# Kernel optimization log

Hardware: AMD Instinct MI355X
Metric: run time of the kernel (lower is better)

The kernel has to match this reference:

```python
import jax, jax.numpy as jnp
import numpy as np

WS = 8
HEADS = 12


def _dwconv(x, w, b):
    # x: (N, C, H, W); w: (C, 1, 3, 3) depthwise, zero pad 1
    y = jax.lax.conv_general_dilated(
        x, w, window_strides=(1, 1), padding=((1, 1), (1, 1)),
        dimension_numbers=("NCHW", "OIHW", "NCHW"), feature_group_count=x.shape[1])
    return y + b[None, :, None, None]


def _sepconv(x, dw, db, pw, pb):
    y = _dwconv(x, dw, db)
    # pointwise 1x1 conv: (N,C,H,W) x (O,C) -> (N,O,H,W)
    return jnp.einsum("nchw,oc->nohw", y, pw) + pb[None, :, None, None]


def _rel_pos_index(ws):
    coords = np.stack(np.meshgrid(np.arange(ws), np.arange(ws), indexing="ij"))  # (2, ws, ws)
    cf = coords.reshape(2, -1)
    rel = cf[:, :, None] - cf[:, None, :]          # (2, ws*ws, ws*ws)
    rel = rel.transpose(1, 2, 0).copy()
    rel[..., 0] += ws - 1
    rel[..., 1] += ws - 1
    rel[..., 0] *= 2 * ws - 1
    return rel.sum(-1)                             # (ws*ws, ws*ws)


def setup_inputs() -> dict:
    key = jax.random.key(0)
    ks = jax.random.split(key, 16)
    B, T, C, H, W = 2, 1, 384, 192, 192
    s = 0.02
    inp = {
        "vid": jax.random.normal(ks[0], (B, T, C, H, W), jnp.float32),
        "qd_w": jax.random.normal(ks[1], (C, 1, 3, 3), jnp.float32) * s,
        "qd_b": jnp.zeros((C,), jnp.float32),
        "qp_w": jax.random.normal(ks[2], (C, C), jnp.float32) * s,
        "qp_b": jnp.zeros((C,), jnp.float32),
        "kd_w": jax.random.normal(ks[3], (C, 1, 3, 3), jnp.float32) * s,
        "kd_b": jnp.zeros((C,), jnp.float32),
        "kp_w": jax.random.normal(ks[4], (C, C), jnp.float32) * s,
        "kp_b": jnp.zeros((C,), jnp.float32),
        "vd_w": jax.random.normal(ks[5], (C, 1, 3, 3), jnp.float32) * s,
        "vd_b": jnp.zeros((C,), jnp.float32),
        "vp_w": jax.random.normal(ks[6], (C, C), jnp.float32) * s,
        "vp_b": jnp.zeros((C,), jnp.float32),
        "rpb_table": jax.random.normal(ks[7], ((2 * WS - 1) ** 2, HEADS), jnp.float32) * s,
        "proj_w": jax.random.normal(ks[8], (C, C), jnp.float32) * s,
        "proj_b": jnp.zeros((C,), jnp.float32),
    }
    return inp


def reference(vid, qd_w, qd_b, qp_w, qp_b, kd_w, kd_b, kp_w, kp_b,
              vd_w, vd_b, vp_w, vp_b, rpb_table, proj_w, proj_b):
    B, T, C, H, W = vid.shape
    heads, ws = HEADS, WS
    hd = C // heads
    scale = hd ** -0.5
    x = vid.reshape(B * T, C, H, W)

    q = _sepconv(x, qd_w, qd_b, qp_w, qp_b) * scale
    k = _sepconv(x, kd_w, kd_b, kp_w, kp_b)
    v = _sepconv(x, vd_w, vd_b, vp_w, vp_b)

    nh, nw = H // ws, W // ws

    def win(z):  # (N, C, H, W) -> (N*nh*nw, heads, ws*ws, hd)
        N = z.shape[0]
        z = z.reshape(N, heads, hd, nh, ws, nw, ws)
        z = z.transpose(0, 3, 5, 1, 4, 6, 2)  # N, nh, nw, heads, ws, ws, hd
        return z.reshape(N * nh * nw, heads, ws * ws, hd)

    qw, kw, vw = win(q), win(k), win(v)

    # product search within window (dists = q . k), rel-pos bias softmax
    attn = jnp.einsum("nhqd,nhkd->nhqk", qw, kw)
    rp_idx = _rel_pos_index(ws)  # static (64, 64)
    bias = rpb_table[rp_idx.reshape(-1)].reshape(ws * ws, ws * ws, heads)
    bias = bias.transpose(2, 0, 1)  # (heads, 64, 64)
    attn = jax.nn.softmax(attn + bias[None], axis=-1)

    # weighted patch sum (ps=1 -> pixels)
    out = jnp.einsum("nhqk,nhkd->nhqd", attn, vw)  # (N*nh*nw, heads, ws*ws, hd)

    # un-window, merge heads into (h c) channel order, then token projection
    out = out.reshape(B * T, nh, nw, heads, ws, ws, hd)
    out = out.transpose(0, 1, 4, 2, 5, 3, 6).reshape(B * T, H, W, heads * hd)
    out = out @ proj_w.T + proj_b

    # fold (ps=1, stride0=1): identity overlap-add, zvid == 1
    out = out.transpose(0, 3, 1, 2).reshape(B, T, C, H, W)
    return out
```

## Files before the change

kernel.cpp:

```cpp
#include <hip/hip_runtime.h>

#define CCH 384
#define HH 192
#define WWD 192
#define NIMG 2
#define HWP (HH * WWD)
#define PTOT (NIMG * HWP)
#define HEADS 12
#define HD 32
#define NWIN 24
#define WINS 576
#define EELEM ((size_t)NIMG * CCH * HWP)
#define WMAT 147456

typedef __attribute__((ext_vector_type(8))) short bh8;
typedef __attribute__((ext_vector_type(8))) unsigned short us8;
typedef __attribute__((ext_vector_type(4))) unsigned short us4;
typedef __attribute__((ext_vector_type(4))) float fx4;

__device__ __forceinline__ unsigned short f2bf(float f) {
    unsigned u = __float_as_uint(f);
    u += 0x7fffu + ((u >> 16) & 1u);
    return (unsigned short)(u >> 16);
}

__device__ __forceinline__ void gload16(const void* g, void* l) {
    __builtin_amdgcn_global_load_lds(
        (const __attribute__((address_space(1))) void*)g,
        (__attribute__((address_space(3))) void*)l, 16, 0, 0);
}

__global__ __launch_bounds__(256) void prep(
    const float* __restrict__ qp, const float* __restrict__ kp,
    const float* __restrict__ vp, const float* __restrict__ pj,
    const float* __restrict__ qd, const float* __restrict__ kd,
    const float* __restrict__ vd, const float* __restrict__ rpb,
    unsigned short* __restrict__ Wb, float* __restrict__ dwT,
    float* __restrict__ Bx)
{
    int bx = blockIdx.x;
    if (bx < 288) {
        int idx8 = (bx * 256 + threadIdx.x) * 8;
        int which = idx8 / WMAT;
        int loc = idx8 - which * WMAT;
        const float* s = (which == 0) ? qp : (which == 1) ? kp : (which == 2) ? vp : pj;
        float4 v0 = *(const float4*)(s + loc);
        float4 v1 = *(const float4*)(s + loc + 4);
        us8 ov;
        ov[0] = f2bf(v0.x); ov[1] = f2bf(v0.y); ov[2] = f2bf(v0.z); ov[3] = f2bf(v0.w);
        ov[4] = f2bf(v1.x); ov[5] = f2bf(v1.y); ov[6] = f2bf(v1.z); ov[7] = f2bf(v1.w);
        *(us8*)(Wb + idx8) = ov;
    } else if (bx < 329) {
        int idx = (bx - 288) * 256 + threadIdx.x;
        if (idx < 3 * 9 * CCH) {
            int ten = idx / (9 * CCH);
            int rem = idx - ten * (9 * CCH);
            int tap = rem / CCH;
            int c   = rem - tap * CCH;
            const float* s = (ten == 0) ? qd : (ten == 1) ? kd : vd;
            dwT[idx] = s[c * 9 + tap];
        }
    } else {
        int idx = (bx - 329) * 256 + threadIdx.x;
        int h  = idx >> 12;
        int tk = (idx >> 6) & 63;
        int tq = idx & 63;
        int dy = (tq >> 3) - (tk >> 3) + 7;
        int dx = (tq & 7) - (tk & 7) + 7;
        Bx[idx] = rpb[(dy * 15 + dx) * HEADS + h];
    }
}

__global__ __launch_bounds__(256) void dwgather(
    const float* __restrict__ x,
    const float* __restrict__ wt,
    const float* __restrict__ qb, const float* __restrict__ kb,
    const float* __restrict__ vb,
    unsigned short* __restrict__ oq, unsigned short* __restrict__ ok,
    unsigned short* __restrict__ ov)
{
    __shared__ float halo[64 * 121];

    int bid = blockIdx.x;
    int b = (bid & 7) * 864 + (bid >> 3);
    int wtx  = b % 24;
    int strip = b / 24;
    int chv  = strip % 6;
    int nwy  = strip / 6;
    int wy   = nwy % 24;
    int n    = nwy / 24;

    int h0 = wy * 8, w0 = wtx * 8;
    int tid = threadIdx.x;
    int c   = tid & 63;
    int pxg = tid >> 6;
    int cg  = chv * 64 + c;
    int widx = n * WINS + wy * NWIN + wtx;

    const float* xbase = x + (size_t)n * CCH * HWP + (size_t)(chv * 64) * HWP;

    for (int j = tid; j < 1920; j += 256) {
        int seg = j % 3;
        int t   = j / 3;
        int rr  = t % 10;
        int cc  = t / 10;
        int hr  = h0 - 1 + rr;
        int cb  = w0 - 2 + seg * 4;
        float4 val = make_float4(0.f, 0.f, 0.f, 0.f);
        if (hr >= 0 && hr < HH) {
            const float* p = xbase + (size_t)cc * HWP + (size_t)hr * WWD;
            if (cb >= 0 && cb + 4 <= WWD) {
                val = *(const float4*)(p + cb);
            } else {
                if (cb + 0 >= 0 && cb + 0 < WWD) val.x = p[cb + 0];
                if (cb + 1 >= 0 && cb + 1 < WWD) val.y = p[cb + 1];
                if (cb + 2 >= 0 && cb + 2 < WWD) val.z = p[cb + 2];
                if (cb + 3 >= 0 && cb + 3 < WWD) val.w = p[cb + 3];
            }
        }
        int hb = cc * 121 + rr * 12 + seg * 4;
        halo[hb + 0] = val.x;
        halo[hb + 1] = val.y;
        halo[hb + 2] = val.z;
        halo[hb + 3] = val.w;
    }

    float wq[9], wk[9], wv[9];
#pragma unroll
    for (int t = 0; t < 9; ++t) {
        wq[t] = wt[t * CCH + cg];
        wk[t] = wt[9 * CCH + t * CCH + cg];
        wv[t] = wt[18 * CCH + t * CCH + cg];
    }
    float bqv = qb[cg], bkv = kb[cg], bvv = vb[cg];

    __syncthreads();

    const int hbase = c * 121 + (2 * pxg) * 12;
    float r0[10], r1[10], r2[10];
#pragma unroll
    for (int cc = 0; cc < 10; ++cc) r0[cc] = halo[hbase + cc + 1];
#pragma unroll
    for (int cc = 0; cc < 10; ++cc) r1[cc] = halo[hbase + 12 + cc + 1];
#pragma unroll
    for (int cc = 0; cc < 10; ++cc) r2[cc] = halo[hbase + 24 + cc + 1];

    size_t ob0 = ((size_t)widx * 64 + pxg * 16) * CCH + cg;

#pragma unroll
    for (int pc = 0; pc < 8; ++pc) {
        float sq = 0.f, sk = 0.f, sv = 0.f;
#pragma unroll
        for (int dc = 0; dc < 3; ++dc) {
            float x0 = r0[pc + dc], x1 = r1[pc + dc], x2 = r2[pc + dc];
            sq = fmaf(x0, wq[dc], sq);     sk = fmaf(x0, wk[dc], sk);     sv = fmaf(x0, wv[dc], sv);
            sq = fmaf(x1, wq[3 + dc], sq); sk = fmaf(x1, wk[3 + dc], sk); sv = fmaf(x1, wv[3 + dc], sv);
            sq = fmaf(x2, wq[6 + dc], sq); sk = fmaf(x2, wk[6 + dc], sk); sv = fmaf(x2, wv[6 + dc], sv);
        }
        size_t o = ob0 + (size_t)pc * CCH;
        oq[o] = f2bf(sq + bqv);
        ok[o] = f2bf(sk + bkv);
        ov[o] = f2bf(sv + bvv);
    }

#pragma unroll
    for (int cc = 0; cc < 10; ++cc) r0[cc] = halo[hbase + 36 + cc + 1];

#pragma unroll
    for (int pc = 0; pc < 8; ++pc) {
        float sq = 0.f, sk = 0.f, sv = 0.f;
#pragma unroll
        for (int dc = 0; dc < 3; ++dc) {
            float x0 = r1[pc + dc], x1 = r2[pc + dc], x2 = r0[pc + dc];
            sq = fmaf(x0, wq[dc], sq);     sk = fmaf(x0, wk[dc], sk);     sv = fmaf(x0, wv[dc], sv);
            sq = fmaf(x1, wq[3 + dc], sq); sk = fmaf(x1, wk[3 + dc], sk); sv = fmaf(x1, wv[3 + dc], sv);
            sq = fmaf(x2, wq[6 + dc], sq); sk = fmaf(x2, wk[6 + dc], sk); sv = fmaf(x2, wv[6 + dc], sv);
        }
        size_t o = ob0 + (size_t)(8 + pc) * CCH;
        oq[o] = f2bf(sq + bqv);
        ok[o] = f2bf(sk + bkv);
        ov[o] = f2bf(sv + bvv);
    }
}

template<int ORIENT>
__global__ __launch_bounds__(256) void pw_gemm(
    const unsigned short* __restrict__ Y, const unsigned short* __restrict__ Wb,
    const float* __restrict__ bias, float scale,
    unsigned short* __restrict__ outb, float* __restrict__ outf)
{
    __shared__ __align__(16) char smem[33792];
    typedef unsigned short (*tile3)[128][32];
    tile3 Wt = (tile3)smem;
    tile3 Yt = (tile3)(smem + 16384);
    typedef unsigned short (*tep_t)[132];
    tep_t T16 = (tep_t)smem;

    int tid = threadIdx.x;
    int pp0 = blockIdx.x * 128;
    int cm0 = blockIdx.y * 128;
    int lid = tid & 63, wid = tid >> 6;
    int wr = wid >> 1, wc = wid & 1;
    int li = lid & 15, g = lid >> 4;

    int srow = (lid >> 2);
    int scol = (lid & 3) * 8;

    fx4 acc[4][4];
#pragma unroll
    for (int i = 0; i < 4; ++i)
#pragma unroll
        for (int j = 0; j < 4; ++j) acc[i][j] = (fx4){0.f, 0.f, 0.f, 0.f};

    tile3 A3 = (ORIENT == 1) ? Wt : Yt;
    tile3 B3 = (ORIENT == 1) ? Yt : Wt;

    const unsigned short* Wg0 = Wb + (size_t)(cm0 + wid * 32 + srow) * CCH + scol;
    const unsigned short* Yg0 = Y  + (size_t)(pp0 + wid * 32 + srow) * CCH + scol;

#pragma unroll
    for (int qi = 0; qi < 2; ++qi) {
        gload16(Wg0 + (size_t)qi * 16 * CCH, &Wt[0][wid * 32 + qi * 16][0]);
        gload16(Yg0 + (size_t)qi * 16 * CCH, &Yt[0][wid * 32 + qi * 16][0]);
    }
    __syncthreads();

    for (int kt = 0; kt < 12; ++kt) {
        int cur = kt & 1;
        if (kt < 11) {
            int k1 = (kt + 1) * 32;
#pragma unroll
            for (int qi = 0; qi < 2; ++qi) {
                gload16(Wg0 + (size_t)qi * 16 * CCH + k1, &Wt[cur ^ 1][wid * 32 + qi * 16][0]);
                gload16(Yg0 + (size_t)qi * 16 * CCH + k1, &Yt[cur ^ 1][wid * 32 + qi * 16][0]);
            }
        }

        bh8 a[4], b[4];
#pragma unroll
        for (int mf = 0; mf < 4; ++mf)
            a[mf] = *(const bh8*)&A3[cur][wr * 64 + mf * 16 + li][g * 8];
#pragma unroll
        for (int nf = 0; nf < 4; ++nf)
            b[nf] = *(const bh8*)&B3[cur][wc * 64 + nf * 16 + li][g * 8];
#pragma unroll
        for (int mf = 0; mf < 4; ++mf)
#pragma unroll
            for (int nf = 0; nf < 4; ++nf)
                acc[mf][nf] = __builtin_amdgcn_mfma_f32_16x16x32_bf16(
                    a[mf], b[nf], acc[mf][nf], 0, 0, 0);

        __syncthreads();
    }

    if (ORIENT == 1) {
#pragma unroll
        for (int mf = 0; mf < 4; ++mf) {
            int cl = wr * 64 + mf * 16 + g * 4;
            float4 bv = *(const float4*)&bias[cm0 + cl];
#pragma unroll
            for (int nf = 0; nf < 4; ++nf) {
                int pl = wc * 64 + nf * 16 + li;
                us4 o;
                o[0] = f2bf((acc[mf][nf][0] + bv.x) * scale);
                o[1] = f2bf((acc[mf][nf][1] + bv.y) * scale);
                o[2] = f2bf((acc[mf][nf][2] + bv.z) * scale);
                o[3] = f2bf((acc[mf][nf][3] + bv.w) * scale);
                *(us4*)&T16[pl][cl] = o;
            }
        }
        __syncthreads();
#pragma unroll
        for (int it = 0; it < 8; ++it) {
            int row = it * 16 + wid * 4 + (lid >> 4);
            int col = (lid & 15) * 8;
            us8 vv = *(const us8*)&T16[row][col];
            *(us8*)(outb + (size_t)(pp0 + row) * CCH + cm0 + col) = vv;
        }
    } else if (ORIENT == 2) {
#pragma unroll
        for (int nf = 0; nf < 4; ++nf) {
            int cl = wc * 64 + nf * 16 + li;
            float bv = bias[cm0 + cl];
#pragma unroll
            for (int mf = 0; mf < 4; ++mf) {
                int pl = wr * 64 + mf * 16 + g * 4;
                us4 o;
                o[0] = f2bf(acc[mf][nf][0] + bv);
                o[1] = f2bf(acc[mf][nf][1] + bv);
                o[2] = f2bf(acc[mf][nf][2] + bv);
                o[3] = f2bf(acc[mf][nf][3] + bv);
                *(us4*)&T16[cl][pl] = o;
            }
        }
        __syncthreads();
        int n = pp0 / HWP;
        int pl0 = pp0 - n * HWP;
#pragma unroll
        for (int it = 0; it < 8; ++it) {
            int row = it * 16 + wid * 4 + (lid >> 4);
            int col = (lid & 15) * 8;
            us8 vv = *(const us8*)&T16[row][col];
            *(us8*)(outb + (size_t)(n * CCH + cm0 + row) * HWP + pl0 + col) = vv;
        }
    } else {
#pragma unroll
        for (int nf = 0; nf < 4; ++nf) {
            int c = cm0 + wc * 64 + nf * 16 + li;
            float bv = bias[c];
#pragma unroll
            for (int mf = 0; mf < 4; ++mf) {
                int p = pp0 + wr * 64 + mf * 16 + g * 4;
                int n = p / HWP;
                int rem = p - n * HWP;
                int win = rem >> 6, t = rem & 63;
                int h = (win / NWIN) * 8 + (t >> 3);
                int w = (win % NWIN) * 8 + (t & 7);
                float4 o;
                o.x = acc[mf][nf][0] + bv;
                o.y = acc[mf][nf][1] + bv;
                o.z = acc[mf][nf][2] + bv;
                o.w = acc[mf][nf][3] + bv;
                *(float4*)(outf + (size_t)(n * CCH + c) * HWP + h * WWD + w) = o;
            }
        }
    }
}

__global__ __launch_bounds__(256) void attn(
    const unsigned short* __restrict__ q, const unsigned short* __restrict__ k,
    const unsigned short* __restrict__ v, const float* __restrict__ Bx,
    unsigned short* __restrict__ o)
{
    __shared__ unsigned short Pl[4][64][72];

    int tid = threadIdx.x, lid = tid & 63, wid = tid >> 6;
    int wl = blockIdx.x;
    int n = wl / WINS, winl = wl - n * WINS;
    int li = lid & 15, g = lid >> 4;

    const fx4 z = (fx4){0.f, 0.f, 0.f, 0.f};

    for (int hq = wid; hq < HEADS; hq += 4) {
        const unsigned short* qp = q + (size_t)(wl * 64) * CCH + hq * HD + g * 8;
        const unsigned short* kp = k + (size_t)(wl * 64) * CCH + hq * HD + g * 8;
        bh8 aq[4], bk[4];
#pragma unroll
        for (int mf = 0; mf < 4; ++mf)
            aq[mf] = *(const bh8*)(qp + (size_t)(mf * 16 + li) * CCH);
#pragma unroll
        for (int nf = 0; nf < 4; ++nf)
            bk[nf] = *(const bh8*)(kp + (size_t)(nf * 16 + li) * CCH);

        fx4 s[4][4];
#pragma unroll
        for (int mf = 0; mf < 4; ++mf)
#pragma unroll
            for (int nf = 0; nf < 4; ++nf)
                s[mf][nf] = __builtin_amdgcn_mfma_f32_16x16x32_bf16(aq[mf], bk[nf], z, 0, 0, 0);

#pragma unroll
        for (int mf = 0; mf < 4; ++mf)
#pragma unroll
            for (int nf = 0; nf < 4; ++nf) {
                fx4 bv = *(const fx4*)&Bx[((size_t)hq * 64 + nf * 16 + li) * 64
                                          + mf * 16 + g * 4];
                s[mf][nf] += bv;
            }

        float inv_[4][4];
#pragma unroll
        for (int mf = 0; mf < 4; ++mf)
#pragma unroll
            for (int r = 0; r < 4; ++r) {
                float m = s[mf][0][r];
#pragma unroll
                for (int nf = 1; nf < 4; ++nf) m = fmaxf(m, s[mf][nf][r]);
                m = fmaxf(m, __shfl_xor(m, 1));
                m = fmaxf(m, __shfl_xor(m, 2));
                m = fmaxf(m, __shfl_xor(m, 4));
                m = fmaxf(m, __shfl_xor(m, 8));
                float sum = 0.f;
#pragma unroll
                for (int nf = 0; nf < 4; ++nf) {
                    float e = __expf(s[mf][nf][r] - m);
                    s[mf][nf][r] = e;
                    sum += e;
                }
                sum += __shfl_xor(sum, 1);
                sum += __shfl_xor(sum, 2);
                sum += __shfl_xor(sum, 4);
                sum += __shfl_xor(sum, 8);
                inv_[mf][r] = 1.f / sum;
            }

#pragma unroll
        for (int mf = 0; mf < 4; ++mf)
#pragma unroll
            for (int nf = 0; nf < 4; ++nf)
#pragma unroll
                for (int r = 0; r < 4; ++r)
                    Pl[wid][mf * 16 + g * 4 + r][nf * 16 + li] =
                        f2bf(s[mf][nf][r] * inv_[mf][r]);

        fx4 o2[2][4];
#pragma unroll
        for (int m2 = 0; m2 < 2; ++m2)
#pragma unroll
            for (int nf = 0; nf < 4; ++nf) o2[m2][nf] = z;
#pragma unroll
        for (int ks = 0; ks < 2; ++ks) {
            bh8 av[2], bp[4];
#pragma unroll
            for (int m2 = 0; m2 < 2; ++m2)
                av[m2] = *(const bh8*)(v + (size_t)(n * CCH + hq * HD + m2 * 16 + li) * HWP
                                         + winl * 64 + ks * 32 + g * 8);
#pragma unroll
            for (int nf = 0; nf < 4; ++nf)
                bp[nf] = *(const bh8*)&Pl[wid][nf * 16 + li][ks * 32 + g * 8];
#pragma unroll
            for (int m2 = 0; m2 < 2; ++m2)
#pragma unroll
                for (int nf = 0; nf < 4; ++nf)
                    o2[m2][nf] = __builtin_amdgcn_mfma_f32_16x16x32_bf16(
                        av[m2], bp[nf], o2[m2][nf], 0, 0, 0);
        }
#pragma unroll
        for (int nf = 0; nf < 4; ++nf) {
            int tq = nf * 16 + li;
#pragma unroll
            for (int m2 = 0; m2 < 2; ++m2) {
                int d = hq * HD + m2 * 16 + g * 4;
                us4 ov;
                ov[0] = f2bf(o2[m2][nf][0]);
                ov[1] = f2bf(o2[m2][nf][1]);
                ov[2] = f2bf(o2[m2][nf][2]);
                ov[3] = f2bf(o2[m2][nf][3]);
                *(us4*)(o + (size_t)(wl * 64 + tq) * CCH + d) = ov;
            }
        }
    }
}

extern "C" void kernel_launch(void* const* d_in, const int* in_sizes, int n_in,
                              void* d_out, int out_size, void* d_ws, size_t ws_size,
                              hipStream_t stream) {
    const float* vid  = (const float*)d_in[0];
    const float* qd_w = (const float*)d_in[1];
    const float* qd_b = (const float*)d_in[2];
    const float* qp_w = (const float*)d_in[3];
    const float* qp_b = (const float*)d_in[4];
    const float* kd_w = (const float*)d_in[5];
    const float* kd_b = (const float*)d_in[6];
    const float* kp_w = (const float*)d_in[7];
    const float* kp_b = (const float*)d_in[8];
    const float* vd_w = (const float*)d_in[9];
    const float* vd_b = (const float*)d_in[10];
    const float* vp_w = (const float*)d_in[11];
    const float* vp_b = (const float*)d_in[12];
    const float* rpb  = (const float*)d_in[13];
    const float* pj_w = (const float*)d_in[14];
    const float* pj_b = (const float*)d_in[15];

    unsigned short* ws16 = (unsigned short*)d_ws;
    unsigned short* tr0 = ws16 + 3 * EELEM;
    unsigned short* tr1 = ws16 + 4 * EELEM;
    unsigned short* tr2 = ws16 + 5 * EELEM;
    unsigned short* Wb  = ws16 + 6 * EELEM;
    float* dwT          = (float*)(Wb + 4 * WMAT);
    float* Bx           = dwT + 3 * 9 * CCH;
    unsigned short* qb  = ws16;
    unsigned short* kb  = ws16 + EELEM;
    unsigned short* vb  = ws16 + 2 * EELEM;
    unsigned short* ob  = tr0;

    prep<<<521, 256, 0, stream>>>(qp_w, kp_w, vp_w, pj_w,
                                  qd_w, kd_w, vd_w, rpb, Wb, dwT, Bx);
    dwgather<<<NIMG * WINS * 6, 256, 0, stream>>>(
        vid, dwT, qd_b, kd_b, vd_b, tr0, tr1, tr2);

    dim3 gg(PTOT / 128, 3);
    const float scale = 0.17677669529663687f;
    pw_gemm<1><<<gg, 256, 0, stream>>>(tr0, Wb,             qp_b, scale, qb, nullptr);
    pw_gemm<1><<<gg, 256, 0, stream>>>(tr1, Wb + WMAT,      kp_b, 1.0f,  kb, nullptr);
    pw_gemm<2><<<gg, 256, 0, stream>>>(tr2, Wb + 2 * WMAT,  vp_b, 1.0f,  vb, nullptr);

    attn<<<NIMG * WINS, 256, 0, stream>>>(qb, kb, vb, Bx, ob);

    pw_gemm<3><<<gg, 256, 0, stream>>>(ob, Wb + 3 * WMAT, pj_b, 1.0f, nullptr, (float*)d_out);
}
```

Measured before the change: 405.4 us.

## Merge QKV GEMMs into one launch, halve dwgather channel tile, retarget proj epilogue

The three Q/K/V pointwise GEMM launches are merged into a single launch that uses a z grid dimension and picks inputs per block, which removes launch gaps and lets the three GEMMs overlap. The depthwise gather kernel now handles 32 channels and 8 pixel rows per block, doubling the block count and halving shared memory per block to raise occupancy, at the cost of more halo reloads across blocks. The output projection gets its own kernel with swapped operand roles, so each lane writes scalar fp32 values strided by channel instead of float4 rows, changing the write coalescing pattern.

Result: slower. 420.6 us (+3.8%).

```diff
diff --git a/kernel.cpp b/kernel.cpp
--- a/kernel.cpp
+++ b/kernel.cpp
@@ -79,27 +79,27 @@
     unsigned short* __restrict__ oq, unsigned short* __restrict__ ok,
     unsigned short* __restrict__ ov)
 {
-    __shared__ float halo[64 * 121];
+    __shared__ float halo[32 * 121];
 
     int bid = blockIdx.x;
-    int b = (bid & 7) * 864 + (bid >> 3);
+    int b = (bid & 7) * 1728 + (bid >> 3);
     int wtx  = b % 24;
-    int strip = b / 24;
-    int chv  = strip % 6;
-    int nwy  = strip / 6;
+    int rest = b / 24;
+    int chv  = rest % 12;
+    int nwy  = rest / 12;
     int wy   = nwy % 24;
     int n    = nwy / 24;
 
     int h0 = wy * 8, w0 = wtx * 8;
     int tid = threadIdx.x;
-    int c   = tid & 63;
-    int pxg = tid >> 6;
-    int cg  = chv * 64 + c;
+    int c   = tid & 31;
+    int pxg = tid >> 5;
+    int cg  = chv * 32 + c;
     int widx = n * WINS + wy * NWIN + wtx;
 
-    const float* xbase = x + (size_t)n * CCH * HWP + (size_t)(chv * 64) * HWP;
-
-    for (int j = tid; j < 1920; j += 256) {
+    const float* xbase = x + (size_t)n * CCH * HWP + (size_t)(chv * 32) * HWP;
+
+    for (int j = tid; j < 960; j += 256) {
         int seg = j % 3;
         int t   = j / 3;
         int rr  = t % 10;
@@ -136,7 +136,7 @@
 
     __syncthreads();
 
-    const int hbase = c * 121 + (2 * pxg) * 12;
+    const int hbase = c * 121 + pxg * 12;
     float r0[10], r1[10], r2[10];
 #pragma unroll
     for (int cc = 0; cc < 10; ++cc) r0[cc] = halo[hbase + cc + 1];
@@ -145,7 +145,7 @@
 #pragma unroll
     for (int cc = 0; cc < 10; ++cc) r2[cc] = halo[hbase + 24 + cc + 1];
 
-    size_t ob0 = ((size_t)widx * 64 + pxg * 16) * CCH + cg;
+    size_t ob0 = ((size_t)widx * 64 + pxg * 8) * CCH + cg;
 
 #pragma unroll
     for (int pc = 0; pc < 8; ++pc) {
@@ -162,32 +162,15 @@
         ok[o] = f2bf(sk + bkv);
         ov[o] = f2bf(sv + bvv);
     }
-
-#pragma unroll
-    for (int cc = 0; cc < 10; ++cc) r0[cc] = halo[hbase + 36 + cc + 1];
-
-#pragma unroll
-    for (int pc = 0; pc < 8; ++pc) {
-        float sq = 0.f, sk = 0.f, sv = 0.f;
-#pragma unroll
-        for (int dc = 0; dc < 3; ++dc) {
-            float x0 = r1[pc + dc], x1 = r2[pc + dc], x2 = r0[pc + dc];
-            sq = fmaf(x0, wq[dc], sq);     sk = fmaf(x0, wk[dc], sk);     sv = fmaf(x0, wv[dc], sv);
-            sq = fmaf(x1, wq[3 + dc], sq); sk = fmaf(x1, wk[3 + dc], sk); sv = fmaf(x1, wv[3 + dc], sv);
-            sq = fmaf(x2, wq[6 + dc], sq); sk = fmaf(x2, wk[6 + dc], sk); sv = fmaf(x2, wv[6 + dc], sv);
-        }
-        size_t o = ob0 + (size_t)(8 + pc) * CCH;
-        oq[o] = f2bf(sq + bqv);
-        ok[o] = f2bf(sk + bkv);
-        ov[o] = f2bf(sv + bvv);
-    }
-}
-
-template<int ORIENT>
-__global__ __launch_bounds__(256) void pw_gemm(
-    const unsigned short* __restrict__ Y, const unsigned short* __restrict__ Wb,
-    const float* __restrict__ bias, float scale,
-    unsigned short* __restrict__ outb, float* __restrict__ outf)
+}
+
+__global__ __launch_bounds__(256) void qkv_gemm(
+    const unsigned short* __restrict__ tr0, const unsigned short* __restrict__ tr1,
+    const unsigned short* __restrict__ tr2, const unsigned short* __restrict__ Wball,
+    const float* __restrict__ qpb, const float* __restrict__ kpb,
+    const float* __restrict__ vpb, float scale,
+    unsigned short* __restrict__ qo, unsigned short* __restrict__ ko,
+    unsigned short* __restrict__ vo)
 {
     __shared__ __align__(16) char smem[33792];
     typedef unsigned short (*tile3)[128][32];
@@ -196,6 +179,14 @@
     typedef unsigned short (*tep_t)[132];
     tep_t T16 = (tep_t)smem;
 
+    int z = blockIdx.z;
+    const unsigned short* Y  = (z == 0) ? tr0 : (z == 1) ? tr1 : tr2;
+    const unsigned short* Wb = Wball + (size_t)z * WMAT;
+    const float* bias        = (z == 0) ? qpb : (z == 1) ? kpb : vpb;
+    float sc                 = (z == 0) ? scale : 1.0f;
+    unsigned short* outb     = (z == 0) ? qo : (z == 1) ? ko : vo;
+    bool vmode = (z == 2);
+
     int tid = threadIdx.x;
     int pp0 = blockIdx.x * 128;
     int cm0 = blockIdx.y * 128;
@@ -212,8 +203,8 @@
 #pragma unroll
         for (int j = 0; j < 4; ++j) acc[i][j] = (fx4){0.f, 0.f, 0.f, 0.f};
 
-    tile3 A3 = (ORIENT == 1) ? Wt : Yt;
-    tile3 B3 = (ORIENT == 1) ? Yt : Wt;
+    tile3 A3 = vmode ? Yt : Wt;
+    tile3 B3 = vmode ? Wt : Yt;
 
     const unsigned short* Wg0 = Wb + (size_t)(cm0 + wid * 32 + srow) * CCH + scol;
     const unsigned short* Yg0 = Y  + (size_t)(pp0 + wid * 32 + srow) * CCH + scol;
@@ -253,7 +244,7 @@
         __syncthreads();
     }
 
-    if (ORIENT == 1) {
+    if (!vmode) {
 #pragma unroll
         for (int mf = 0; mf < 4; ++mf) {
             int cl = wr * 64 + mf * 16 + g * 4;
@@ -262,10 +253,10 @@
             for (int nf = 0; nf < 4; ++nf) {
                 int pl = wc * 64 + nf * 16 + li;
                 us4 o;
-                o[0] = f2bf((acc[mf][nf][0] + bv.x) * scale);
-                o[1] = f2bf((acc[mf][nf][1] + bv.y) * scale);
-                o[2] = f2bf((acc[mf][nf][2] + bv.z) * scale);
-                o[3] = f2bf((acc[mf][nf][3] + bv.w) * scale);
+                o[0] = f2bf((acc[mf][nf][0] + bv.x) * sc);
+                o[1] = f2bf((acc[mf][nf][1] + bv.y) * sc);
+                o[2] = f2bf((acc[mf][nf][2] + bv.z) * sc);
+                o[3] = f2bf((acc[mf][nf][3] + bv.w) * sc);
                 *(us4*)&T16[pl][cl] = o;
             }
         }
@@ -277,7 +268,7 @@
             us8 vv = *(const us8*)&T16[row][col];
             *(us8*)(outb + (size_t)(pp0 + row) * CCH + cm0 + col) = vv;
         }
-    } else if (ORIENT == 2) {
+    } else {
 #pragma unroll
         for (int nf = 0; nf < 4; ++nf) {
             int cl = wc * 64 + nf * 16 + li;
@@ -303,26 +294,85 @@
             us8 vv = *(const us8*)&T16[row][col];
             *(us8*)(outb + (size_t)(n * CCH + cm0 + row) * HWP + pl0 + col) = vv;
         }
-    } else {
+    }
+}
+
+__global__ __launch_bounds__(256) void proj_gemm(
+    const unsigned short* __restrict__ Y, const unsigned short* __restrict__ Wb,
+    const float* __restrict__ bias, float* __restrict__ outf)
+{
+    __shared__ unsigned short Wt[2][128][32];
+    __shared__ unsigned short Yt[2][128][32];
+
+    int tid = threadIdx.x;
+    int pp0 = blockIdx.x * 128;
+    int cm0 = blockIdx.y * 128;
+    int lid = tid & 63, wid = tid >> 6;
+    int wr = wid >> 1, wc = wid & 1;
+    int li = lid & 15, g = lid >> 4;
+
+    int srow = (lid >> 2);
+    int scol = (lid & 3) * 8;
+
+    fx4 acc[4][4];
+#pragma unroll
+    for (int i = 0; i < 4; ++i)
+#pragma unroll
+        for (int j = 0; j < 4; ++j) acc[i][j] = (fx4){0.f, 0.f, 0.f, 0.f};
+
+    const unsigned short* Wg0 = Wb + (size_t)(cm0 + wid * 32 + srow) * CCH + scol;
+    const unsigned short* Yg0 = Y  + (size_t)(pp0 + wid * 32 + srow) * CCH + scol;
+
+#pragma unroll
+    for (int qi = 0; qi < 2; ++qi) {
+        gload16(Wg0 + (size_t)qi * 16 * CCH, &Wt[0][wid * 32 + qi * 16][0]);
+        gload16(Yg0 + (size_t)qi * 16 * CCH, &Yt[0][wid * 32 + qi * 16][0]);
+    }
+    __syncthreads();
+
+    for (int kt = 0; kt < 12; ++kt) {
+        int cur = kt & 1;
+        if (kt < 11) {
+            int k1 = (kt + 1) * 32;
+#pragma unroll
+            for (int qi = 0; qi < 2; ++qi) {
+                gload16(Wg0 + (size_t)qi * 16 * CCH + k1, &Wt[cur ^ 1][wid * 32 + qi * 16][0]);
+                gload16(Yg0 + (size_t)qi * 16 * CCH + k1, &Yt[cur ^ 1][wid * 32 + qi * 16][0]);
+            }
+        }
+
+        bh8 a[4], b[4];
+#pragma unroll
+        for (int mf = 0; mf < 4; ++mf)
+            a[mf] = *(const bh8*)&Wt[cur][wr * 64 + mf * 16 + li][g * 8];
+#pragma unroll
+        for (int nf = 0; nf < 4; ++nf)
+            b[nf] = *(const bh8*)&Yt[cur][wc * 64 + nf * 16 + li][g * 8];
+#pragma unroll
+        for (int mf = 0; mf < 4; ++mf)
+#pragma unroll
+            for (int nf = 0; nf < 4; ++nf)
+                acc[mf][nf] = __builtin_amdgcn_mfma_f32_16x16x32_bf16(
+                    a[mf], b[nf], acc[mf][nf], 0, 0, 0);
+
+        __syncthreads();
+    }
+
+#pragma unroll
+    for (int mf = 0; mf < 4; ++mf) {
+        int c = cm0 + wr * 64 + mf * 16 + g * 4;
 #pragma unroll
         for (int nf = 0; nf < 4; ++nf) {
-            int c = cm0 + wc * 64 + nf * 16 + li;
-            float bv = bias[c];
-#pragma unroll
-            for (int mf = 0; mf < 4; ++mf) {
-                int p = pp0 + wr * 64 + mf * 16 + g * 4;
-                int n = p / HWP;
-                int rem = p - n * HWP;
-                int win = rem >> 6, t = rem & 63;
-                int h = (win / NWIN) * 8 + (t >> 3);
-                int w = (win % NWIN) * 8 + (t & 7);
-                float4 o;
-                o.x = acc[mf][nf][0] + bv;
-                o.y = acc[mf][nf][1] + bv;
-                o.z = acc[mf][nf][2] + bv;
-                o.w = acc[mf][nf][3] + bv;
-                *(float4*)(outf + (size_t)(n * CCH + c) * HWP + h * WWD + w) = o;
-            }
+            int p = pp0 + wc * 64 + nf * 16 + li;
+            int n = p / HWP;
+            int rem = p - n * HWP;
+            int win = rem >> 6, t = rem & 63;
+            int h = (win / NWIN) * 8 + (t >> 3);
+            int w = (win % NWIN) * 8 + (t & 7);
+            float* op = outf + (size_t)n * CCH * HWP + (size_t)h * WWD + w;
+#pragma unroll
+            for (int r = 0; r < 4; ++r)
+                op[(size_t)(c + r) * HWP] = acc[mf][nf][r] + bias[c + r];
         }
     }
 }
@@ -476,16 +526,15 @@
 
     prep<<<521, 256, 0, stream>>>(qp_w, kp_w, vp_w, pj_w,
                                   qd_w, kd_w, vd_w, rpb, Wb, dwT, Bx);
-    dwgather<<<NIMG * WINS * 6, 256, 0, stream>>>(
+    dwgather<<<NIMG * WINS * 12, 256, 0, stream>>>(
         vid, dwT, qd_b, kd_b, vd_b, tr0, tr1, tr2);
 
-    dim3 gg(PTOT / 128, 3);
     const float scale = 0.17677669529663687f;
-    pw_gemm<1><<<gg, 256, 0, stream>>>(tr0, Wb,             qp_b, scale, qb, nullptr);
-    pw_gemm<1><<<gg, 256, 0, stream>>>(tr1, Wb + WMAT,      kp_b, 1.0f,  kb, nullptr);
-    pw_gemm<2><<<gg, 256, 0, stream>>>(tr2, Wb + 2 * WMAT,  vp_b, 1.0f,  vb, nullptr);
+    qkv_gemm<<<dim3(PTOT / 128, 3, 3), 256, 0, stream>>>(
+        tr0, tr1, tr2, Wb, qp_b, kp_b, vp_b, scale, qb, kb, vb);
 
     attn<<<NIMG * WINS, 256, 0, stream>>>(qb, kb, vb, Bx, ob);
 
-    pw_gemm<3><<<gg, 256, 0, stream>>>(ob, Wb + 3 * WMAT, pj_b, 1.0f, nullptr, (float*)d_out);
-}
+    proj_gemm<<<dim3(PTOT / 128, 3), 256, 0, stream>>>(
+        ob, Wb + 3 * WMAT, pj_b, (float*)d_out);
+}
```
